# Optimization experiments

Hardware: AMD Instinct MI355X
Metric: run time of the kernel (lower is better)

The kernel has to match this reference:

```python
import jax, jax.numpy as jnp
import numpy as np

EMBED_DIM = 1024
NUM_HEADS = 16
HEAD_DIM = EMBED_DIM // NUM_HEADS


def setup_inputs() -> dict:
    key = jax.random.key(0)
    ks = jax.random.split(key, 6)
    s = 1.0 / np.sqrt(EMBED_DIM)
    x = jax.random.normal(ks[0], (2, 2048, EMBED_DIM), dtype=jnp.float32)
    Wk = jax.random.uniform(ks[1], (EMBED_DIM, EMBED_DIM), jnp.float32, -s, s)
    Wq = jax.random.uniform(ks[2], (EMBED_DIM, EMBED_DIM), jnp.float32, -s, s)
    Wv = jax.random.uniform(ks[3], (EMBED_DIM, EMBED_DIM), jnp.float32, -s, s)
    Wo = jax.random.uniform(ks[4], (EMBED_DIM, EMBED_DIM), jnp.float32, -s, s)
    bo = jax.random.uniform(ks[5], (EMBED_DIM,), jnp.float32, -s, s)
    return {"x": x, "Wq": Wq, "Wk": Wk, "Wv": Wv, "Wo": Wo, "bo": bo}


def reference(x, Wq, Wk, Wv, Wo, bo):
    b, s, e = x.shape
    h, d = NUM_HEADS, HEAD_DIM
    scale = d ** (-0.5)
    # nn.Linear: y = x @ W.T ; here W stored as [out, in] -> use W.T
    q = (x @ Wq.T).reshape(b, s, h, d).transpose(0, 2, 1, 3)  # b h s d
    k = (x @ Wk.T).reshape(b, s, h, d).transpose(0, 2, 1, 3)
    v = (x @ Wv.T).reshape(b, s, h, d).transpose(0, 2, 1, 3)
    logits = jnp.einsum('bhqd,bhkd->bhqk', q, k) * scale
    attn = jax.nn.softmax(logits, axis=-1)
    out = jnp.einsum('bhqk,bhkd->bhqd', attn, v)
    out = out.transpose(0, 2, 1, 3).reshape(b, s, e)
    return out @ Wo.T + bo
```

## Files before the change

### kernel.cpp

```cpp
#include <hip/hip_runtime.h>
#include <hip/hip_bf16.h>

using short8 = __attribute__((ext_vector_type(8))) short;
using f32x4  = __attribute__((ext_vector_type(4))) float;
using uint4v = __attribute__((ext_vector_type(4))) unsigned;

#if __has_builtin(__builtin_amdgcn_exp2f)
#define EXP2(x) __builtin_amdgcn_exp2f(x)
#else
#define EXP2(x) exp2f(x)
#endif

__device__ __forceinline__ short f2bf(float f) {
    union { float f; unsigned u; } v; v.f = f;
    unsigned r = v.u + 0x7fffu + ((v.u >> 16) & 1u);
    return (short)(r >> 16);
}
__device__ __forceinline__ unsigned pack_trunc(float a, float b) {
    union { float f; unsigned u; } ua, ub; ua.f = a; ub.f = b;
#if __has_builtin(__builtin_amdgcn_perm)
    return __builtin_amdgcn_perm(ub.u, ua.u, 0x07060302u);
#else
    return (ub.u & 0xFFFF0000u) | (ua.u >> 16);
#endif
}
__device__ __forceinline__ void async_copy16(const short* g, short* s) {
    __builtin_amdgcn_global_load_lds(
        (const __attribute__((address_space(1))) void*)g,
        (__attribute__((address_space(3))) void*)s, 16, 0, 0);
}

__global__ __launch_bounds__(256) void cvt_f32_bf16(
    const float* __restrict__ s0, const float* __restrict__ s1,
    const float* __restrict__ s2, const float* __restrict__ s3,
    const float* __restrict__ s4,
    short* __restrict__ d0, short* __restrict__ d1, short* __restrict__ d2,
    short* __restrict__ d3, short* __restrict__ d4) {
    const int bid = blockIdx.x;
    const float* s; short* d; int base;
    if (bid < 4096) {
        s = s0; d = d0; base = bid << 10;
    } else {
        const int r = bid - 4096;
        base = (r & 1023) << 10;
        switch (r >> 10) {
            case 0: s = s1; d = d1; break;
            case 1: s = s2; d = d2; break;
            case 2: s = s3; d = d3; break;
            default: s = s4; d = d4; break;
        }
    }
    const int idx = base + threadIdx.x * 4;
    float4 v = *(const float4*)(s + idx);
    short4 o;
    o.x = f2bf(v.x); o.y = f2bf(v.y); o.z = f2bf(v.z); o.w = f2bf(v.w);
    *(short4*)(d + idx) = o;
}

template <int MODE>
__device__ __forceinline__ void gemm_body(const short* __restrict__ A,
                                          const short* __restrict__ B,
                                          short* __restrict__ C,
                                          float scale,
                                          short* __restrict__ As,
                                          short* __restrict__ Bs) {
    constexpr int Kd = 1024, Nd = 1024, Sd = 2048;

    const int tid  = threadIdx.x;
    const int w    = tid >> 6, lane = tid & 63;
    const int quad = lane >> 4, l16 = lane & 15;
    const int xr   = l16 & 7;
    const int wm   = (w >> 1) * 64, wn = (w & 1) * 64;
    const int bm   = blockIdx.y * 128, bn = blockIdx.x * 128;

    f32x4 acc[4][4];
#pragma unroll
    for (int i = 0; i < 4; ++i)
#pragma unroll
        for (int j = 0; j < 4; ++j) acc[i][j] = (f32x4){0.f, 0.f, 0.f, 0.f};

    for (int k0 = 0; k0 < Kd; k0 += 64) {
        __syncthreads();
#pragma unroll
        for (int c = 0; c < 4; ++c) {
            int li   = c * 256 + tid;
            int row  = li >> 3;
            int gcol = ((li & 7) ^ (row & 7)) * 8;
            async_copy16(A + (size_t)(bm + row) * Kd + k0 + gcol, &As[li * 8]);
            async_copy16(B + (size_t)(bn + row) * Kd + k0 + gcol, &Bs[li * 8]);
        }
        __syncthreads();

#pragma unroll
        for (int kk = 0; kk < 2; ++kk) {
            short8 af[4], bfv[4];
#pragma unroll
            for (int mi = 0; mi < 4; ++mi) {
                const int r = wm + mi * 16 + l16;
                af[mi] = *(const short8*)(
                    &As[r * 64 + (((kk * 4 + quad) ^ xr) * 8)]);
            }
#pragma unroll
            for (int ni = 0; ni < 4; ++ni) {
                const int r = wn + ni * 16 + l16;
                bfv[ni] = *(const short8*)(
                    &Bs[r * 64 + (((kk * 4 + quad) ^ xr) * 8)]);
            }
#pragma unroll
            for (int mi = 0; mi < 4; ++mi)
#pragma unroll
                for (int ni = 0; ni < 4; ++ni) {
                    if constexpr (MODE == 2)
                        acc[mi][ni] = __builtin_amdgcn_mfma_f32_16x16x32_bf16(
                            bfv[ni], af[mi], acc[mi][ni], 0, 0, 0);
                    else
                        acc[mi][ni] = __builtin_amdgcn_mfma_f32_16x16x32_bf16(
                            af[mi], bfv[ni], acc[mi][ni], 0, 0, 0);
                }
        }
    }

    if constexpr (MODE == 2) {
#pragma unroll
        for (int mi = 0; mi < 4; ++mi) {
            const int m_g = bm + wm + mi * 16 + l16;
            const int b_  = m_g >> 11, s_ = m_g & 2047;
#pragma unroll
            for (int ni = 0; ni < 4; ++ni)
#pragma unroll
                for (int r = 0; r < 4; ++r) {
                    const int n_g = bn + wn + ni * 16 + quad * 4 + r;
                    C[(size_t)b_ * Nd * Sd + (size_t)n_g * Sd + s_] =
                        f2bf(acc[mi][ni][r]);
                }
        }
    } else {
#pragma unroll
        for (int ni = 0; ni < 4; ++ni) {
            const int colg = bn + wn + ni * 16 + l16;
#pragma unroll
            for (int mi = 0; mi < 4; ++mi)
#pragma unroll
                for (int r = 0; r < 4; ++r) {
                    const int rowg = bm + wm + mi * 16 + quad * 4 + r;
                    C[(size_t)rowg * Nd + colg] = f2bf(acc[mi][ni][r] * scale);
                }
        }
    }
}

#define CSC 0.18033688f

__global__ __launch_bounds__(256, 3) void proj_gemm(
    const short* __restrict__ X,
    const short* __restrict__ Wq, const short* __restrict__ Wk,
    const short* __restrict__ Wv,
    short* __restrict__ Qo, short* __restrict__ Ko, short* __restrict__ VTo) {
    __shared__ __align__(16) short As[128 * 64];
    __shared__ __align__(16) short Bs[128 * 64];
    if (blockIdx.z == 0)
        gemm_body<0>(X, Wq, Qo, CSC, As, Bs);
    else if (blockIdx.z == 1)
        gemm_body<0>(X, Wk, Ko, 1.0f, As, Bs);
    else
        gemm_body<2>(X, Wv, VTo, 1.0f, As, Bs);
}

__global__ __launch_bounds__(256, 2) void out_gemm(
    const short* __restrict__ A, const short* __restrict__ B,
    const float* __restrict__ bias, float* __restrict__ C) {
    constexpr int Kd = 1024, Nd = 1024;
    __shared__ __align__(16) short As[64 * 64];
    __shared__ __align__(16) short Bs[128 * 64];

    const int tid  = threadIdx.x;
    const int w    = tid >> 6, lane = tid & 63;
    const int quad = lane >> 4, l16 = lane & 15;
    const int xr   = l16 & 7;
    const int wm   = (w >> 1) * 32, wn = (w & 1) * 64;
    const int bm   = blockIdx.y * 64, bn = blockIdx.x * 128;

    f32x4 acc[2][4];
#pragma unroll
    for (int i = 0; i < 2; ++i)
#pragma unroll
        for (int j = 0; j < 4; ++j) acc[i][j] = (f32x4){0.f, 0.f, 0.f, 0.f};

    for (int k0 = 0; k0 < Kd; k0 += 64) {
        __syncthreads();
#pragma unroll
        for (int c = 0; c < 2; ++c) {
            int li   = c * 256 + tid;
            int row  = li >> 3;
            int gcol = ((li & 7) ^ (row & 7)) * 8;
            async_copy16(A + (size_t)(bm + row) * Kd + k0 + gcol, &As[li * 8]);
        }
#pragma unroll
        for (int c = 0; c < 4; ++c) {
            int li   = c * 256 + tid;
            int row  = li >> 3;
            int gcol = ((li & 7) ^ (row & 7)) * 8;
            async_copy16(B + (size_t)(bn + row) * Kd + k0 + gcol, &Bs[li * 8]);
        }
        __syncthreads();

#pragma unroll
        for (int kk = 0; kk < 2; ++kk) {
            short8 af[2], bfv[4];
#pragma unroll
            for (int mi = 0; mi < 2; ++mi) {
                const int r = wm + mi * 16 + l16;
                af[mi] = *(const short8*)(
                    &As[r * 64 + (((kk * 4 + quad) ^ xr) * 8)]);
            }
#pragma unroll
            for (int ni = 0; ni < 4; ++ni) {
                const int r = wn + ni * 16 + l16;
                bfv[ni] = *(const short8*)(
                    &Bs[r * 64 + (((kk * 4 + quad) ^ xr) * 8)]);
            }
#pragma unroll
            for (int mi = 0; mi < 2; ++mi)
#pragma unroll
                for (int ni = 0; ni < 4; ++ni)
                    acc[mi][ni] = __builtin_amdgcn_mfma_f32_16x16x32_bf16(
                        af[mi], bfv[ni], acc[mi][ni], 0, 0, 0);
        }
    }

#pragma unroll
    for (int ni = 0; ni < 4; ++ni) {
        const int colg = bn + wn + ni * 16 + l16;
        const float bv = bias[colg];
#pragma unroll
        for (int mi = 0; mi < 2; ++mi)
#pragma unroll
            for (int r = 0; r < 4; ++r) {
                const int rowg = bm + wm + mi * 16 + quad * 4 + r;
                C[(size_t)rowg * Nd + colg] = acc[mi][ni][r] + bv;
            }
    }
}

__global__ __launch_bounds__(256, 2) void attn_kernel(
    const short* __restrict__ Q, const short* __restrict__ K,
    const short* __restrict__ VT, short* __restrict__ O) {
    constexpr int S = 2048, E = 1024, NT = S / 64;
    __shared__ __align__(16) short Ks[2][64 * 64];
    __shared__ __align__(16) short Vs[2][64 * 64];

    const int tid  = threadIdx.x;
    const int w    = tid >> 6, lane = tid & 63;
    const int quad = lane >> 4, l16 = lane & 15;

    const int bid  = blockIdx.x;
    const int xcd  = bid & 7, slot = bid >> 3;
    const int qt   = slot & 15;
    const int bh   = xcd + ((slot >> 4) << 3);
    const int b    = bh >> 4, h = bh & 15;

    const int    q0   = qt * 128 + w * 32;
    const size_t base = (size_t)b * S * E;
    const size_t vtb  = (size_t)b * E * S;
    const int    hc   = h * 64;
    const int    xr   = l16 & 7;

    short8 aq[2][2];
#pragma unroll
    for (int qg = 0; qg < 2; ++qg) {
        const short* qp = Q + base + (size_t)(q0 + qg * 16 + l16) * E + hc + quad * 8;
        aq[qg][0] = *(const short8*)(qp);
        aq[qg][1] = *(const short8*)(qp + 32);
    }

    f32x4 oT[2][4], o_sum[2];
#pragma unroll
    for (int qg = 0; qg < 2; ++qg) {
        o_sum[qg] = (f32x4){0.f, 0.f, 0.f, 0.f};
#pragma unroll
        for (int i = 0; i < 4; ++i) oT[qg][i] = (f32x4){0.f, 0.f, 0.f, 0.f};
    }

    int          kdst[2], vdst0[2], vdst1[2];
    const short* kga[2];
    const short* vga[2];
#pragma unroll
    for (int c = 0; c < 2; ++c) {
        int li = c * 256 + tid, row = li >> 3, cc = li & 7;
        kdst[c] = row * 64 + ((cc ^ (row & 7)) * 8);
        int c0   = 4 * (cc >> 2) + 2 * (cc & 1);
        int boff = 4 * ((cc >> 1) & 1);
        vdst0[c] = row * 64 + ((c0 ^ (row & 7)) * 8) + boff;
        vdst1[c] = row * 64 + (((c0 + 1) ^ (row & 7)) * 8) + boff;
        kga[c]   = K + base + (size_t)row * E + hc + cc * 8;
        vga[c]   = VT + vtb + (size_t)(hc + row) * S + cc * 8;
    }

    short8 krA[2], vrA[2], krB[2], vrB[2];

    auto load_regs = [&](short8* krX, short8* vrX, int t) {
#pragma unroll
        for (int c = 0; c < 2; ++c) {
            krX[c] = *(const short8*)(kga[c] + (size_t)t * 64 * E);
            vrX[c] = *(const short8*)(vga[c] + t * 64);
        }
    };
    auto store_regs = [&](short* Kn, short* Vn, const short8* krX,
                          const short8* vrX) {
#pragma unroll
        for (int c = 0; c < 2; ++c) {
            *(short8*)(&Kn[kdst[c]]) = krX[c];
            short4 lo, hi;
            lo.x = vrX[c][0]; lo.y = vrX[c][1]; lo.z = vrX[c][2]; lo.w = vrX[c][3];
            hi.x = vrX[c][4]; hi.y = vrX[c][5]; hi.z = vrX[c][6]; hi.w = vrX[c][7];
            *(short4*)(&Vn[vdst0[c]]) = lo;
            *(short4*)(&Vn[vdst1[c]]) = hi;
        }
    };

    const short8 ones = (short8){0x3F80, 0x3F80, 0x3F80, 0x3F80,
                                 0x3F80, 0x3F80, 0x3F80, 0x3F80};
    const float  LB   = 0.00281502f;

    auto compute_tile = [&](const short* Kc, const short* Vc) {
        __builtin_amdgcn_s_setprio(1);
        uint4v pkv[2][2];
#pragma unroll
        for (int kn = 0; kn < 4; ++kn) {
            const short* kb  = &Kc[(kn * 16 + l16) * 64];
            short8       bk0 = *(const short8*)(kb + ((quad ^ xr) * 8));
            short8       bk1 = *(const short8*)(kb + (((quad + 4) ^ xr) * 8));
#pragma unroll
            for (int qg = 0; qg < 2; ++qg) {
                f32x4 a = (f32x4){LB, LB, LB, LB};
                a = __builtin_amdgcn_mfma_f32_16x16x32_bf16(bk0, aq[qg][0], a, 0, 0, 0);
                a = __builtin_amdgcn_mfma_f32_16x16x32_bf16(bk1, aq[qg][1], a, 0, 0, 0);
                pkv[qg][kn >> 1][(kn & 1) * 2]     = pack_trunc(EXP2(a[0]), EXP2(a[1]));
                pkv[qg][kn >> 1][(kn & 1) * 2 + 1] = pack_trunc(EXP2(a[2]), EXP2(a[3]));
            }
        }

#pragma unroll
        for (int ks = 0; ks < 2; ++ks) {
            short8 pf[2];
#pragma unroll
            for (int qg = 0; qg < 2; ++qg) {
                union { uint4v u; short8 s; } cv;
                cv.u   = pkv[qg][ks];
                pf[qg] = cv.s;
                o_sum[qg] = __builtin_amdgcn_mfma_f32_16x16x32_bf16(
                    ones, pf[qg], o_sum[qg], 0, 0, 0);
            }
#pragma unroll
            for (int ni = 0; ni < 4; ++ni) {
                const int rv = ni * 16 + l16;
                short8 vb =
                    *(const short8*)(&Vc[rv * 64 + (((ks * 4 + quad) ^ xr) * 8)]);
#pragma unroll
                for (int qg = 0; qg < 2; ++qg)
                    oT[qg][ni] = __builtin_amdgcn_mfma_f32_16x16x32_bf16(
                        vb, pf[qg], oT[qg][ni], 0, 0, 0);
            }
        }
        __builtin_amdgcn_s_setprio(0);
    };

    load_regs(krA, vrA, 0);
    store_regs(Ks[0], Vs[0], krA, vrA);
    load_regs(krA, vrA, 1);
    load_regs(krB, vrB, 2);
    __syncthreads();

#pragma unroll 1
    for (int kt = 0; kt < NT; kt += 2) {
        store_regs(Ks[1], Vs[1], krA, vrA);
        if (kt + 3 < NT) load_regs(krA, vrA, kt + 3);
        compute_tile(Ks[0], Vs[0]);
        __syncthreads();

        if (kt + 2 < NT) store_regs(Ks[0], Vs[0], krB, vrB);
        if (kt + 4 < NT) load_regs(krB, vrB, kt + 4);
        compute_tile(Ks[1], Vs[1]);
        __syncthreads();
    }

#pragma unroll
    for (int qg = 0; qg < 2; ++qg) {
        const float inv = 1.0f / o_sum[qg][0];
        const int   qg_ = q0 + qg * 16 + l16;
#pragma unroll
        for (int ni = 0; ni < 4; ++ni) {
            short4 ov;
            ov.x = f2bf(oT[qg][ni][0] * inv);
            ov.y = f2bf(oT[qg][ni][1] * inv);
            ov.z = f2bf(oT[qg][ni][2] * inv);
            ov.w = f2bf(oT[qg][ni][3] * inv);
            *(short4*)(&O[base + (size_t)qg_ * E + hc + ni * 16 + quad * 4]) = ov;
        }
    }
}

extern "C" void kernel_launch(void* const* d_in, const int* in_sizes, int n_in,
                              void* d_out, int out_size, void* d_ws, size_t ws_size,
                              hipStream_t stream) {
    const float* x  = (const float*)d_in[0];
    const float* Wq = (const float*)d_in[1];
    const float* Wk = (const float*)d_in[2];
    const float* Wv = (const float*)d_in[3];
    const float* Wo = (const float*)d_in[4];
    const float* bo = (const float*)d_in[5];
    float* out = (float*)d_out;

    constexpr int XN = 2 * 2048 * 1024;
    constexpr int WN = 1024 * 1024;

    short* Xb  = (short*)d_ws;
    short* Wqb = Xb + XN;
    short* Wkb = Wqb + WN;
    short* Wvb = Wkb + WN;
    short* Wob = Wvb + WN;
    short* Qb  = Wob + WN;
    short* Kb  = Qb + XN;
    short* VTb = Kb + XN;

    cvt_f32_bf16<<<dim3(8192), 256, 0, stream>>>(
        x, Wq, Wk, Wv, Wo, Xb, Wqb, Wkb, Wvb, Wob);
    proj_gemm<<<dim3(8, 32, 3), 256, 0, stream>>>(Xb, Wqb, Wkb, Wvb, Qb, Kb, VTb);
    attn_kernel<<<dim3(512), 256, 0, stream>>>(Qb, Kb, VTb, Xb );
    out_gemm<<<dim3(8, 64), 256, 0, stream>>>(Xb, Wob, bo, out);
}
```

Measured before the change: 171.2 us.

## Double attention KV tile to 128 keys with simpler one-ahead prefetch

The attention kernel now processes 128 keys per shared-memory tile instead of 64, which halves the number of barriers per sweep. The register prefetch changes from two tiles ahead (A/B sets) to one tile ahead with a single register set. Compute is restructured so that each 32-key chunk computes QK, exp and PV together, which limits the live P registers. In exchange, LDS use per block doubles to 64KB and each thread holds larger staging registers, which may lower occupancy, and prefetch distance in keys stays similar.

```diff
diff --git a/kernel.cpp b/kernel.cpp
--- a/kernel.cpp
+++ b/kernel.cpp
@@ -245,9 +245,9 @@
 __global__ __launch_bounds__(256, 2) void attn_kernel(
     const short* __restrict__ Q, const short* __restrict__ K,
     const short* __restrict__ VT, short* __restrict__ O) {
-    constexpr int S = 2048, E = 1024, NT = S / 64;
-    __shared__ __align__(16) short Ks[2][64 * 64];
-    __shared__ __align__(16) short Vs[2][64 * 64];
+    constexpr int S = 2048, E = 1024, KV = 128, NT = S / KV;
+    __shared__ __align__(16) short Ks[2][KV * 64];
+    __shared__ __align__(16) short Vs[2][64 * KV];
 
     const int tid  = threadIdx.x;
     const int w    = tid >> 6, lane = tid & 63;
@@ -281,38 +281,42 @@
         for (int i = 0; i < 4; ++i) oT[qg][i] = (f32x4){0.f, 0.f, 0.f, 0.f};
     }
 
-    int          kdst[2], vdst0[2], vdst1[2];
-    const short* kga[2];
-    const short* vga[2];
-#pragma unroll
-    for (int c = 0; c < 2; ++c) {
-        int li = c * 256 + tid, row = li >> 3, cc = li & 7;
-        kdst[c] = row * 64 + ((cc ^ (row & 7)) * 8);
-        int c0   = 4 * (cc >> 2) + 2 * (cc & 1);
-        int boff = 4 * ((cc >> 1) & 1);
-        vdst0[c] = row * 64 + ((c0 ^ (row & 7)) * 8) + boff;
-        vdst1[c] = row * 64 + (((c0 + 1) ^ (row & 7)) * 8) + boff;
-        kga[c]   = K + base + (size_t)row * E + hc + cc * 8;
-        vga[c]   = VT + vtb + (size_t)(hc + row) * S + cc * 8;
-    }
-
-    short8 krA[2], vrA[2], krB[2], vrB[2];
-
-    auto load_regs = [&](short8* krX, short8* vrX, int t) {
-#pragma unroll
-        for (int c = 0; c < 2; ++c) {
-            krX[c] = *(const short8*)(kga[c] + (size_t)t * 64 * E);
-            vrX[c] = *(const short8*)(vga[c] + t * 64);
+    int          kdst[4], vdst0[4], vdst1[4];
+    const short* kga[4];
+    const short* vga[4];
+#pragma unroll
+    for (int c = 0; c < 4; ++c) {
+        const int li = c * 256 + tid;
+        {
+            const int row = li >> 3, cc = li & 7;
+            kdst[c] = row * 64 + ((cc ^ (row & 7)) * 8);
+            kga[c]  = K + base + (size_t)row * E + hc + cc * 8;
+        }
+        {
+            const int row = li >> 4, cc = li & 15;
+            const int c0   = 4 * (cc >> 2) + 2 * (cc & 1);
+            const int boff = 4 * ((cc >> 1) & 1);
+            vdst0[c] = row * KV + (((c0)     ^ (row & 7)) * 8) + boff;
+            vdst1[c] = row * KV + (((c0 + 1) ^ (row & 7)) * 8) + boff;
+            vga[c]   = VT + vtb + (size_t)(hc + row) * S + cc * 8;
+        }
+    }
+
+    short8 kr[4], vr[4];
+    auto load_regs = [&](int t) {
+#pragma unroll
+        for (int c = 0; c < 4; ++c) {
+            kr[c] = *(const short8*)(kga[c] + (size_t)t * KV * E);
+            vr[c] = *(const short8*)(vga[c] + t * KV);
         }
     };
-    auto store_regs = [&](short* Kn, short* Vn, const short8* krX,
-                          const short8* vrX) {
-#pragma unroll
-        for (int c = 0; c < 2; ++c) {
-            *(short8*)(&Kn[kdst[c]]) = krX[c];
+    auto store_regs = [&](short* Kn, short* Vn) {
+#pragma unroll
+        for (int c = 0; c < 4; ++c) {
+            *(short8*)(&Kn[kdst[c]]) = kr[c];
             short4 lo, hi;
-            lo.x = vrX[c][0]; lo.y = vrX[c][1]; lo.z = vrX[c][2]; lo.w = vrX[c][3];
-            hi.x = vrX[c][4]; hi.y = vrX[c][5]; hi.z = vrX[c][6]; hi.w = vrX[c][7];
+            lo.x = vr[c][0]; lo.y = vr[c][1]; lo.z = vr[c][2]; lo.w = vr[c][3];
+            hi.x = vr[c][4]; hi.y = vr[c][5]; hi.z = vr[c][6]; hi.w = vr[c][7];
             *(short4*)(&Vn[vdst0[c]]) = lo;
             *(short4*)(&Vn[vdst1[c]]) = hi;
         }
@@ -324,29 +328,29 @@
 
     auto compute_tile = [&](const short* Kc, const short* Vc) {
         __builtin_amdgcn_s_setprio(1);
-        uint4v pkv[2][2];
-#pragma unroll
-        for (int kn = 0; kn < 4; ++kn) {
-            const short* kb  = &Kc[(kn * 16 + l16) * 64];
-            short8       bk0 = *(const short8*)(kb + ((quad ^ xr) * 8));
-            short8       bk1 = *(const short8*)(kb + (((quad + 4) ^ xr) * 8));
-#pragma unroll
-            for (int qg = 0; qg < 2; ++qg) {
-                f32x4 a = (f32x4){LB, LB, LB, LB};
-                a = __builtin_amdgcn_mfma_f32_16x16x32_bf16(bk0, aq[qg][0], a, 0, 0, 0);
-                a = __builtin_amdgcn_mfma_f32_16x16x32_bf16(bk1, aq[qg][1], a, 0, 0, 0);
-                pkv[qg][kn >> 1][(kn & 1) * 2]     = pack_trunc(EXP2(a[0]), EXP2(a[1]));
-                pkv[qg][kn >> 1][(kn & 1) * 2 + 1] = pack_trunc(EXP2(a[2]), EXP2(a[3]));
-            }
-        }
-
-#pragma unroll
-        for (int ks = 0; ks < 2; ++ks) {
+#pragma unroll
+        for (int ks = 0; ks < 4; ++ks) {
+            uint4v pkq[2];
+#pragma unroll
+            for (int kh = 0; kh < 2; ++kh) {
+                const int    kn  = ks * 2 + kh;
+                const short* kb  = &Kc[(kn * 16 + l16) * 64];
+                short8       bk0 = *(const short8*)(kb + ((quad ^ xr) * 8));
+                short8       bk1 = *(const short8*)(kb + (((quad + 4) ^ xr) * 8));
+#pragma unroll
+                for (int qg = 0; qg < 2; ++qg) {
+                    f32x4 a = (f32x4){LB, LB, LB, LB};
+                    a = __builtin_amdgcn_mfma_f32_16x16x32_bf16(bk0, aq[qg][0], a, 0, 0, 0);
+                    a = __builtin_amdgcn_mfma_f32_16x16x32_bf16(bk1, aq[qg][1], a, 0, 0, 0);
+                    pkq[qg][kh * 2]     = pack_trunc(EXP2(a[0]), EXP2(a[1]));
+                    pkq[qg][kh * 2 + 1] = pack_trunc(EXP2(a[2]), EXP2(a[3]));
+                }
+            }
             short8 pf[2];
 #pragma unroll
             for (int qg = 0; qg < 2; ++qg) {
                 union { uint4v u; short8 s; } cv;
-                cv.u   = pkv[qg][ks];
+                cv.u   = pkq[qg];
                 pf[qg] = cv.s;
                 o_sum[qg] = __builtin_amdgcn_mfma_f32_16x16x32_bf16(
                     ones, pf[qg], o_sum[qg], 0, 0, 0);
@@ -354,8 +358,8 @@
 #pragma unroll
             for (int ni = 0; ni < 4; ++ni) {
                 const int rv = ni * 16 + l16;
-                short8 vb =
-                    *(const short8*)(&Vc[rv * 64 + (((ks * 4 + quad) ^ xr) * 8)]);
+                short8 vb = *(const short8*)(
+                    &Vc[rv * KV + (((ks * 4 + quad) ^ xr) * 8)]);
 #pragma unroll
                 for (int qg = 0; qg < 2; ++qg)
                     oT[qg][ni] = __builtin_amdgcn_mfma_f32_16x16x32_bf16(
@@ -365,22 +369,19 @@
         __builtin_amdgcn_s_setprio(0);
     };
 
-    load_regs(krA, vrA, 0);
-    store_regs(Ks[0], Vs[0], krA, vrA);
-    load_regs(krA, vrA, 1);
-    load_regs(krB, vrB, 2);
+    load_regs(0);
+    store_regs(Ks[0], Vs[0]);
+    load_regs(1);
     __syncthreads();
 
 #pragma unroll 1
-    for (int kt = 0; kt < NT; kt += 2) {
-        store_regs(Ks[1], Vs[1], krA, vrA);
-        if (kt + 3 < NT) load_regs(krA, vrA, kt + 3);
-        compute_tile(Ks[0], Vs[0]);
-        __syncthreads();
-
-        if (kt + 2 < NT) store_regs(Ks[0], Vs[0], krB, vrB);
-        if (kt + 4 < NT) load_regs(krB, vrB, kt + 4);
-        compute_tile(Ks[1], Vs[1]);
+    for (int kt = 0; kt < NT; ++kt) {
+        const int cur = kt & 1;
+        if (kt + 1 < NT) {
+            store_regs(Ks[cur ^ 1], Vs[cur ^ 1]);
+            if (kt + 2 < NT) load_regs(kt + 2);
+        }
+        compute_tile(Ks[cur], Vs[cur]);
         __syncthreads();
     }
 
```

After: 173.3 us. About the same (+1.2%).

## Software-pipeline attention: interleave PV of previous tile with QK of current tile

Applied to the files above, without the earlier changes.

Restructures the attention inner loop so the P·V products for tile kt-1 are interleaved with the Q·K and exp computation for tile kt, using a triple-buffered V in shared memory and ping-pong P register sets. The goal is to hide exp/pack latency and LDS reads behind independent MFMAs. It drops the second prefetch register set, so only one tile of global loads is in flight at a time. It also raises LDS use with the third V buffer, which may reduce occupancy.

```diff
diff --git a/kernel.cpp b/kernel.cpp
--- a/kernel.cpp
+++ b/kernel.cpp
@@ -247,7 +247,7 @@
     const short* __restrict__ VT, short* __restrict__ O) {
     constexpr int S = 2048, E = 1024, NT = S / 64;
     __shared__ __align__(16) short Ks[2][64 * 64];
-    __shared__ __align__(16) short Vs[2][64 * 64];
+    __shared__ __align__(16) short Vs[3][64 * 64];
 
     const int tid  = threadIdx.x;
     const int w    = tid >> 6, lane = tid & 63;
@@ -296,23 +296,22 @@
         vga[c]   = VT + vtb + (size_t)(hc + row) * S + cc * 8;
     }
 
-    short8 krA[2], vrA[2], krB[2], vrB[2];
-
-    auto load_regs = [&](short8* krX, short8* vrX, int t) {
+    short8 kr[2], vr[2];
+    auto load_regs = [&](int t) {
 #pragma unroll
         for (int c = 0; c < 2; ++c) {
-            krX[c] = *(const short8*)(kga[c] + (size_t)t * 64 * E);
-            vrX[c] = *(const short8*)(vga[c] + t * 64);
+            kr[c] = *(const short8*)(kga[c] + (size_t)t * 64 * E);
+            vr[c] = *(const short8*)(vga[c] + t * 64);
         }
     };
-    auto store_regs = [&](short* Kn, short* Vn, const short8* krX,
-                          const short8* vrX) {
+    auto store_regs = [&](short* Kn, short* Vn) {
 #pragma unroll
         for (int c = 0; c < 2; ++c) {
-            *(short8*)(&Kn[kdst[c]]) = krX[c];
+            *(short8*)(&Kn[kdst[c]]) = kr[c];
             short4 lo, hi;
-            lo.x = vrX[c][0]; lo.y = vrX[c][1]; lo.z = vrX[c][2]; lo.w = vrX[c][3];
-            hi.x = vrX[c][4]; hi.y = vrX[c][5]; hi.z = vrX[c][6]; hi.w = vrX[c][7];
+            lo.x = kr[c][0];
+            lo.x = vr[c][0]; lo.y = vr[c][1]; lo.z = vr[c][2]; lo.w = vr[c][3];
+            hi.x = vr[c][4]; hi.y = vr[c][5]; hi.z = vr[c][6]; hi.w = vr[c][7];
             *(short4*)(&Vn[vdst0[c]]) = lo;
             *(short4*)(&Vn[vdst1[c]]) = hi;
         }
@@ -322,11 +321,12 @@
                                  0x3F80, 0x3F80, 0x3F80, 0x3F80};
     const float  LB   = 0.00281502f;
 
-    auto compute_tile = [&](const short* Kc, const short* Vc) {
-        __builtin_amdgcn_s_setprio(1);
-        uint4v pkv[2][2];
-#pragma unroll
-        for (int kn = 0; kn < 4; ++kn) {
+    uint4v pkvA[2][2], pkvB[2][2];
+
+    auto qk_half = [&](const short* Kc, uint4v (&pc)[2][2], int h) {
+#pragma unroll
+        for (int kh = 0; kh < 2; ++kh) {
+            const int    kn  = h * 2 + kh;
             const short* kb  = &Kc[(kn * 16 + l16) * 64];
             short8       bk0 = *(const short8*)(kb + ((quad ^ xr) * 8));
             short8       bk1 = *(const short8*)(kb + (((quad + 4) ^ xr) * 8));
@@ -335,54 +335,71 @@
                 f32x4 a = (f32x4){LB, LB, LB, LB};
                 a = __builtin_amdgcn_mfma_f32_16x16x32_bf16(bk0, aq[qg][0], a, 0, 0, 0);
                 a = __builtin_amdgcn_mfma_f32_16x16x32_bf16(bk1, aq[qg][1], a, 0, 0, 0);
-                pkv[qg][kn >> 1][(kn & 1) * 2]     = pack_trunc(EXP2(a[0]), EXP2(a[1]));
-                pkv[qg][kn >> 1][(kn & 1) * 2 + 1] = pack_trunc(EXP2(a[2]), EXP2(a[3]));
-            }
-        }
-
-#pragma unroll
-        for (int ks = 0; ks < 2; ++ks) {
-            short8 pf[2];
-#pragma unroll
-            for (int qg = 0; qg < 2; ++qg) {
-                union { uint4v u; short8 s; } cv;
-                cv.u   = pkv[qg][ks];
-                pf[qg] = cv.s;
-                o_sum[qg] = __builtin_amdgcn_mfma_f32_16x16x32_bf16(
-                    ones, pf[qg], o_sum[qg], 0, 0, 0);
-            }
-#pragma unroll
-            for (int ni = 0; ni < 4; ++ni) {
-                const int rv = ni * 16 + l16;
-                short8 vb =
-                    *(const short8*)(&Vc[rv * 64 + (((ks * 4 + quad) ^ xr) * 8)]);
-#pragma unroll
-                for (int qg = 0; qg < 2; ++qg)
-                    oT[qg][ni] = __builtin_amdgcn_mfma_f32_16x16x32_bf16(
-                        vb, pf[qg], oT[qg][ni], 0, 0, 0);
-            }
-        }
+                pc[qg][h][kh * 2]     = pack_trunc(EXP2(a[0]), EXP2(a[1]));
+                pc[qg][h][kh * 2 + 1] = pack_trunc(EXP2(a[2]), EXP2(a[3]));
+            }
+        }
+    };
+    auto pv_half = [&](const short* Vp, uint4v (&pp)[2][2], int ks) {
+        short8 pf[2];
+#pragma unroll
+        for (int qg = 0; qg < 2; ++qg) {
+            union { uint4v u; short8 s; } cv;
+            cv.u   = pp[qg][ks];
+            pf[qg] = cv.s;
+            o_sum[qg] = __builtin_amdgcn_mfma_f32_16x16x32_bf16(
+                ones, pf[qg], o_sum[qg], 0, 0, 0);
+        }
+#pragma unroll
+        for (int ni = 0; ni < 4; ++ni) {
+            const int rv = ni * 16 + l16;
+            short8 vb =
+                *(const short8*)(&Vp[rv * 64 + (((ks * 4 + quad) ^ xr) * 8)]);
+#pragma unroll
+            for (int qg = 0; qg < 2; ++qg)
+                oT[qg][ni] = __builtin_amdgcn_mfma_f32_16x16x32_bf16(
+                    vb, pf[qg], oT[qg][ni], 0, 0, 0);
+        }
+    };
+
+    auto body = [&](int kt, uint4v (&pp)[2][2], uint4v (&pc)[2][2]) {
+        if (kt + 1 < NT) {
+            store_regs(Ks[(kt + 1) & 1], Vs[(kt + 1) % 3]);
+            if (kt + 2 < NT) load_regs(kt + 2);
+        }
+        const short* Kc = Ks[kt & 1];
+        const short* Vp = Vs[(kt - 1) % 3];
+        __builtin_amdgcn_s_setprio(1);
+        pv_half(Vp, pp, 0);
+        qk_half(Kc, pc, 0);
+        pv_half(Vp, pp, 1);
+        qk_half(Kc, pc, 1);
         __builtin_amdgcn_s_setprio(0);
+        __syncthreads();
     };
 
-    load_regs(krA, vrA, 0);
-    store_regs(Ks[0], Vs[0], krA, vrA);
-    load_regs(krA, vrA, 1);
-    load_regs(krB, vrB, 2);
+    load_regs(0);
+    store_regs(Ks[0], Vs[0]);
+    load_regs(1);
     __syncthreads();
+    store_regs(Ks[1], Vs[1]);
+    load_regs(2);
+    __builtin_amdgcn_s_setprio(1);
+    qk_half(Ks[0], pkvA, 0);
+    qk_half(Ks[0], pkvA, 1);
+    __builtin_amdgcn_s_setprio(0);
+    __syncthreads();
 
 #pragma unroll 1
-    for (int kt = 0; kt < NT; kt += 2) {
-        store_regs(Ks[1], Vs[1], krA, vrA);
-        if (kt + 3 < NT) load_regs(krA, vrA, kt + 3);
-        compute_tile(Ks[0], Vs[0]);
-        __syncthreads();
-
-        if (kt + 2 < NT) store_regs(Ks[0], Vs[0], krB, vrB);
-        if (kt + 4 < NT) load_regs(krB, vrB, kt + 4);
-        compute_tile(Ks[1], Vs[1]);
-        __syncthreads();
-    }
+    for (int kt = 1; kt < NT - 1; kt += 2) {
+        body(kt, pkvA, pkvB);
+        body(kt + 1, pkvB, pkvA);
+    }
+    body(NT - 1, pkvA, pkvB);
+    __builtin_amdgcn_s_setprio(1);
+    pv_half(Vs[(NT - 1) % 3], pkvB, 0);
+    pv_half(Vs[(NT - 1) % 3], pkvB, 1);
+    __builtin_amdgcn_s_setprio(0);
 
 #pragma unroll
     for (int qg = 0; qg < 2; ++qg) {
```

Measured after the change: 167.0 us. 1.03x faster.
